# Kernel optimization log

Measured on AMD Instinct MI355X. Metric: run time of the kernel, lower is better.

Reference implementation:

```python
import jax, jax.numpy as jnp
import numpy as np
import math

B, N, T, H, HEADS, FIN, NL_TR = 4, 256, 16, 128, 4, 2, 5
M = B * N
NEG = -1e9

def _sinusoidal(t, h):
    pos = jnp.arange(t, dtype=jnp.float32)[:, None]
    div = jnp.exp(jnp.arange(0, h, 2, dtype=jnp.float32) * (-math.log(10000.0) / h))
    pe = jnp.zeros((t, h), dtype=jnp.float32)
    pe = pe.at[:, 0::2].set(jnp.sin(pos * div))
    pe = pe.at[:, 1::2].set(jnp.cos(pos * div))
    return pe

def _gat(x, W, a_src, a_dst, b, E, m):
    # x: [T,M,F]; W: [F,heads,H]; E: [T,M,M] bool, E[t,i,j]=edge j->i; m: [T,M] bool
    h = jnp.einsum('tmf,fhd->tmhd', x, W)
    ss = jnp.einsum('tmhd,hd->tmh', h, a_src)  # source score per node
    sd = jnp.einsum('tmhd,hd->tmh', h, a_dst)  # dest score per node
    logits = jax.nn.leaky_relu(sd[:, :, None, :] + ss[:, None, :, :], 0.2)  # [T,i,j,h]
    logits = jnp.where(E[..., None], logits, NEG)
    alpha = jax.nn.softmax(logits, axis=2)  # segment-softmax over incoming edges
    out = jnp.einsum('tijh,tjhd->tihd', alpha, h).mean(axis=2) + b  # concat=False -> head mean + bias
    return jax.nn.relu(out) * m[..., None]

def _ln(x, s, b):
    mu = x.mean(-1, keepdims=True)
    v = ((x - mu) ** 2).mean(-1, keepdims=True)
    return (x - mu) / jnp.sqrt(v + 1e-5) * s + b

def _forward(ego_mask, positions, adjacency, gat1_W, gat1_asrc, gat1_adst, gat1_b, gatW, gat_asrc, gat_adst, gat_b, Wqkv, bqkv, Wo, bo, ln1_s, ln1_b, ln2_s, ln2_b, Wff1, bff1, Wff2, bff2):
    m = jnp.transpose(ego_mask, (1, 0, 2)).reshape(T, M)  # [T, B*N]
    eye = jnp.eye(M, dtype=bool)
    # edge j->i valid iff A[t,j,i]!=0 and both nodes masked; PyG GATConv adds self-loops
    E = ((jnp.swapaxes(adjacency, 1, 2) != 0) & m[:, :, None] & m[:, None, :]) | (eye[None] & m[:, :, None])
    x = _gat(positions, gat1_W, gat1_asrc, gat1_adst, gat1_b, E, m)
    for i in range(5):
        x = _gat(x, gatW[i], gat_asrc[i], gat_adst[i], gat_b[i], E, m)
    x_seq = jnp.transpose(x, (1, 0, 2)) + _sinusoidal(T, H)[None]  # [M, T, H]
    dh = H // HEADS
    scale = 1.0 / math.sqrt(dh)
    for l in range(NL_TR):
        q = (x_seq @ Wqkv[l, 0] + bqkv[l, 0]).reshape(M, T, HEADS, dh)
        k = (x_seq @ Wqkv[l, 1] + bqkv[l, 1]).reshape(M, T, HEADS, dh)
        v = (x_seq @ Wqkv[l, 2] + bqkv[l, 2]).reshape(M, T, HEADS, dh)
        sc = jnp.einsum('bqhd,bkhd->bhqk', q, k) * scale
        a = jax.nn.softmax(sc, axis=-1)
        o = jnp.einsum('bhqk,bkhd->bqhd', a, v).reshape(M, T, H) @ Wo[l] + bo[l]
        x_seq = _ln(x_seq + o, ln1_s[l], ln1_b[l])
        f = jax.nn.relu(x_seq @ Wff1[l] + bff1[l]) @ Wff2[l] + bff2[l]
        x_seq = _ln(x_seq + f, ln2_s[l], ln2_b[l])
    return x_seq.reshape(B, N, T, H)

def setup_inputs() -> dict:
    key = jax.random.key(0)
    ks = jax.random.split(key, 32)
    s = 0.05
    f32 = jnp.float32
    inp = {
        'ego_mask': jax.random.uniform(ks[0], (B, T, N)) < 0.95,
        'positions': jax.random.normal(ks[1], (T, M, FIN), dtype=f32),
        'adjacency': (jax.random.uniform(ks[2], (T, M, M)) < 0.02).astype(f32),
        'gat1_W': jax.random.normal(ks[3], (FIN, HEADS, H), dtype=f32) * s,
        'gat1_asrc': jax.random.normal(ks[4], (HEADS, H), dtype=f32) * s,
        'gat1_adst': jax.random.normal(ks[5], (HEADS, H), dtype=f32) * s,
        'gat1_b': jnp.zeros((H,), dtype=f32),
        'gatW': jax.random.normal(ks[6], (5, H, HEADS, H), dtype=f32) * s,
        'gat_asrc': jax.random.normal(ks[7], (5, HEADS, H), dtype=f32) * s,
        'gat_adst': jax.random.normal(ks[8], (5, HEADS, H), dtype=f32) * s,
        'gat_b': jnp.zeros((5, H), dtype=f32),
        'Wqkv': jax.random.normal(ks[9], (NL_TR, 3, H, H), dtype=f32) * s,
        'bqkv': jnp.zeros((NL_TR, 3, H), dtype=f32),
        'Wo': jax.random.normal(ks[10], (NL_TR, H, H), dtype=f32) * s,
        'bo': jnp.zeros((NL_TR, H), dtype=f32),
        'ln1_s': jnp.ones((NL_TR, H), dtype=f32),
        'ln1_b': jnp.zeros((NL_TR, H), dtype=f32),
        'ln2_s': jnp.ones((NL_TR, H), dtype=f32),
        'ln2_b': jnp.zeros((NL_TR, H), dtype=f32),
        'Wff1': jax.random.normal(ks[11], (NL_TR, H, 4 * H), dtype=f32) * s,
        'bff1': jnp.zeros((NL_TR, 4 * H), dtype=f32),
        'Wff2': jax.random.normal(ks[12], (NL_TR, 4 * H, H), dtype=f32) * s,
        'bff2': jnp.zeros((NL_TR, H), dtype=f32),
    }
    return inp

def reference(ego_mask, positions, adjacency, gat1_W, gat1_asrc, gat1_adst, gat1_b, gatW, gat_asrc, gat_adst, gat_b, Wqkv, bqkv, Wo, bo, ln1_s, ln1_b, ln2_s, ln2_b, Wff1, bff1, Wff2, bff2):
    return _forward(ego_mask, positions, adjacency, gat1_W, gat1_asrc, gat1_adst, gat1_b, gatW, gat_asrc, gat_adst, gat_b, Wqkv, bqkv, Wo, bo, ln1_s, ln1_b, ln2_s, ln2_b, Wff1, bff1, Wff2, bff2)
```

## Files before the change

kernel.cpp:

```cpp
#include <hip/hip_runtime.h>
#include <hip/hip_bf16.h>

#define TT 16
#define MM 1024
#define HDIM 128
#define NHEADS 4
#define NROWS (TT*MM)
#define MAXDEG 64

typedef __bf16 bf16x8 __attribute__((ext_vector_type(8)));
typedef float f32x4 __attribute__((ext_vector_type(4)));

__device__ __forceinline__ unsigned short f2b(float x) {
    unsigned u = __float_as_uint(x);
    u += 0x7fff + ((u >> 16) & 1);
    return (unsigned short)(u >> 16);
}
__device__ __forceinline__ float bu2f(unsigned short u) {
    return __uint_as_float(((unsigned)u) << 16);
}
__device__ __forceinline__ void unpk8(uint4 v, float* f) {
    f[0] = bu2f((unsigned short)(v.x & 0xffff)); f[1] = bu2f((unsigned short)(v.x >> 16));
    f[2] = bu2f((unsigned short)(v.y & 0xffff)); f[3] = bu2f((unsigned short)(v.y >> 16));
    f[4] = bu2f((unsigned short)(v.z & 0xffff)); f[5] = bu2f((unsigned short)(v.z >> 16));
    f[6] = bu2f((unsigned short)(v.w & 0xffff)); f[7] = bu2f((unsigned short)(v.w >> 16));
}

__global__ __launch_bounds__(256) void k_init(const int* __restrict__ ego,
                                              float* __restrict__ mfl,
                                              int* __restrict__ cnt) {
    int idx = blockIdx.x * 256 + threadIdx.x;
    int t = idx >> 10, i = idx & 1023;
    int b = i >> 8, n = i & 255;
    mfl[idx] = ego[b * (TT * 256) + t * 256 + n] ? 1.f : 0.f;
    cnt[idx] = 0;
}

__global__ __launch_bounds__(256) void k_edges(const float* __restrict__ adj,
                                               const float* __restrict__ mfl,
                                               int* __restrict__ cnt,
                                               int* __restrict__ nbr) {
    int bid = blockIdx.x;
    int t = bid >> 6, jc = bid & 63;
    int tid = threadIdx.x;
    int i0 = tid * 4;
    int rowb = t * MM;
    float mi[4];
#pragma unroll
    for (int r = 0; r < 4; ++r) mi[r] = mfl[rowb + i0 + r];
    __shared__ float ms[16];
    if (tid < 16) ms[tid] = mfl[rowb + jc * 16 + tid];
    __syncthreads();
    const float* at = adj + (size_t)t * MM * MM;
#pragma unroll 4
    for (int jj = 0; jj < 16; ++jj) {
        int j = jc * 16 + jj;
        float4 a = *(const float4*)(at + (size_t)j * MM + i0);
        float mj = ms[jj];
#pragma unroll
        for (int r = 0; r < 4; ++r) {
            int i = i0 + r;
            bool e;
            if (j == i) e = (mi[r] != 0.f);
            else e = ((&a.x)[r] != 0.f) && (mj != 0.f) && (mi[r] != 0.f);
            if (e) {
                int row = rowb + i;
                int pos = atomicAdd(&cnt[row], 1);
                if (pos < MAXDEG) nbr[(size_t)row * MAXDEG + pos] = j;
            }
        }
    }
}

__global__ __launch_bounds__(256) void k_prep(const float* __restrict__ Wqkv,
                                              const float* __restrict__ Wo,
                                              const float* __restrict__ Wff1,
                                              const float* __restrict__ Wff2,
                                              const float* __restrict__ gW,
                                              unsigned short* __restrict__ Wb) {
    int o = blockIdx.x * 256 + threadIdx.x;
    const float* src; int cs;
    if (o < 122880) {
        int l = o / 24576, r = o % 24576;
        if (r < 6144) {
            int nt = r >> 8, rem = r & 255, ks = rem >> 6, lane = rem & 63;
            int mt = nt >> 3, cc = nt & 7;
            int k = ks * 32 + ((lane >> 4) << 3), c = cc * 16 + (lane & 15);
            src = Wqkv + ((size_t)(l * 3 + mt) * 128 + k) * 128 + c; cs = 128;
        } else if (r < 8192) {
            int u = r - 6144, nt = u >> 8, rem = u & 255, ks = rem >> 6, lane = rem & 63;
            int k = ks * 32 + ((lane >> 4) << 3), c = nt * 16 + (lane & 15);
            src = Wo + (size_t)l * 16384 + (size_t)k * 128 + c; cs = 128;
        } else if (r < 16384) {
            int u = r - 8192, nt = u >> 8, rem = u & 255, ks = rem >> 6, lane = rem & 63;
            int k = ks * 32 + ((lane >> 4) << 3), c = nt * 16 + (lane & 15);
            src = Wff1 + (size_t)l * 65536 + (size_t)k * 512 + c; cs = 512;
        } else {
            int u = r - 16384, nt = u >> 10, rem = u & 1023, ks = rem >> 6, lane = rem & 63;
            int k = ks * 32 + ((lane >> 4) << 3), c = nt * 16 + (lane & 15);
            src = Wff2 + (size_t)l * 65536 + (size_t)k * 128 + c; cs = 128;
        }
    } else {
        int u = o - 122880;
        int l = u >> 13, rr = u & 8191;
        int nt = rr >> 8, rem = rr & 255, ks = rem >> 6, lane = rem & 63;
        int k = ks * 32 + ((lane >> 4) << 3), c = nt * 16 + (lane & 15);
        src = gW + (size_t)l * 65536 + (size_t)k * 512 + c; cs = 512;
    }
    unsigned v[4];
#pragma unroll
    for (int j = 0; j < 4; ++j)
        v[j] = (unsigned)f2b(src[(2 * j) * (size_t)cs]) |
               ((unsigned)f2b(src[(2 * j + 1) * (size_t)cs]) << 16);
    *(uint4*)(Wb + (size_t)o * 8) = make_uint4(v[0], v[1], v[2], v[3]);
}

__global__ __launch_bounds__(128) void k_gat1(const float* __restrict__ x,
                                              const float* __restrict__ W,
                                              const float* __restrict__ asrc,
                                              const float* __restrict__ adst,
                                              unsigned short* __restrict__ h16,
                                              float* __restrict__ ss,
                                              float* __restrict__ sd) {
    int bid = blockIdx.x;
    int row = ((bid & 7) << 11) + (bid >> 3);
    int tid = threadIdx.x;
    float x0 = x[row * 2], x1 = x[row * 2 + 1];
    float s4[4], d4[4];
#pragma unroll
    for (int hh = 0; hh < 4; ++hh) {
        int o = hh * 128 + tid;
        float v = x0 * W[o] + x1 * W[512 + o];
        h16[(size_t)row * 512 + o] = f2b(v);
        s4[hh] = v * asrc[o];
        d4[hh] = v * adst[o];
    }
#pragma unroll
    for (int hh = 0; hh < 4; ++hh)
        for (int off = 32; off; off >>= 1) {
            s4[hh] += __shfl_down(s4[hh], off, 64);
            d4[hh] += __shfl_down(d4[hh], off, 64);
        }
    __shared__ float red[2][2][4];
    if ((tid & 63) == 0) {
        int w = tid >> 6;
#pragma unroll
        for (int hh = 0; hh < 4; ++hh) { red[w][0][hh] = s4[hh]; red[w][1][hh] = d4[hh]; }
    }
    __syncthreads();
    if (tid < 4) ss[row * 4 + tid] = red[0][0][tid] + red[1][0][tid];
    else if (tid < 8) sd[row * 4 + tid - 4] = red[0][1][tid - 4] + red[1][1][tid - 4];
}

__global__ __launch_bounds__(256) void k_gat_h(const unsigned short* __restrict__ x16,
                                               const unsigned short* __restrict__ Wg,
                                               const float* __restrict__ asrc,
                                               const float* __restrict__ adst,
                                               unsigned short* __restrict__ h16,
                                               float* __restrict__ ss,
                                               float* __restrict__ sd) {
    __shared__ __align__(16) unsigned short xb[16 * 136];
    int bid = blockIdx.x;
    int row0 = (((bid & 7) << 7) + (bid >> 3)) * 16;
    int tid = threadIdx.x;
    {
        int rr = tid >> 4, cc = (tid & 15) * 8;
        *(uint4*)(xb + rr * 136 + cc) = *(const uint4*)(x16 + (size_t)(row0 + rr) * 128 + cc);
    }
    __syncthreads();
    const int lane = tid & 63, w = tid >> 6;
    const int mrow = lane & 15, quad = lane >> 4;
    bf16x8 af[4];
#pragma unroll
    for (int ks = 0; ks < 4; ++ks)
        af[ks] = *(const bf16x8*)(xb + mrow * 136 + ks * 32 + quad * 8);
    f32x4 acc[8];
#pragma unroll
    for (int i = 0; i < 8; ++i) acc[i] = (f32x4){0.f, 0.f, 0.f, 0.f};
#pragma unroll
    for (int ib = 0; ib < 4; ++ib) {
        bf16x8 wb[8];
#pragma unroll
        for (int u = 0; u < 2; ++u) {
            int nt = w * 8 + ib * 2 + u;
#pragma unroll
            for (int ks = 0; ks < 4; ++ks)
                wb[u * 4 + ks] = *(const bf16x8*)(Wg + (size_t)((nt * 4 + ks) * 64 + lane) * 8);
        }
#pragma unroll
        for (int u = 0; u < 2; ++u)
#pragma unroll
            for (int ks = 0; ks < 4; ++ks)
                acc[ib * 2 + u] = __builtin_amdgcn_mfma_f32_16x16x32_bf16(af[ks], wb[u * 4 + ks], acc[ib * 2 + u], 0, 0, 0);
    }
    float ps[4] = {0, 0, 0, 0}, pd[4] = {0, 0, 0, 0};
#pragma unroll
    for (int i = 0; i < 8; ++i) {
        int nt = w * 8 + i, col = nt * 16 + mrow;
        float as_ = asrc[col], ad_ = adst[col];
#pragma unroll
        for (int r = 0; r < 4; ++r) {
            float v = acc[i][r];
            h16[(size_t)(row0 + quad * 4 + r) * 512 + col] = f2b(v);
            ps[r] += v * as_; pd[r] += v * ad_;
        }
    }
#pragma unroll
    for (int off = 1; off < 16; off <<= 1)
#pragma unroll
        for (int r = 0; r < 4; ++r) {
            ps[r] += __shfl_xor(ps[r], off, 64);
            pd[r] += __shfl_xor(pd[r], off, 64);
        }
    if (mrow == 0) {
#pragma unroll
        for (int r = 0; r < 4; ++r) {
            int row = row0 + quad * 4 + r;
            ss[row * 4 + w] = ps[r];
            sd[row * 4 + w] = pd[r];
        }
    }
}

__global__ __launch_bounds__(256) void k_agg(const unsigned short* __restrict__ h16,
                                             const float* __restrict__ ss,
                                             const float* __restrict__ sd,
                                             const int* __restrict__ cnt,
                                             const int* __restrict__ nbr,
                                             const float* __restrict__ mfl,
                                             const float* __restrict__ bias,
                                             unsigned short* __restrict__ xo16) {
    int bid = blockIdx.x;
    int row = ((bid & 7) << 11) + (bid >> 3);
    int tid = threadIdx.x;
    int t = row >> 10;
    if (mfl[row] == 0.f) { if (tid < 128) xo16[(size_t)row * 128 + tid] = 0; return; }
    int c = cnt[row]; if (c > MAXDEG) c = MAXDEG;
    __shared__ int nb[MAXDEG];
    __shared__ float al[MAXDEG][4];
    __shared__ __align__(16) float part[1024];
    if (tid < c) nb[tid] = nbr[(size_t)row * MAXDEG + tid];
    __syncthreads();
    for (int idx = tid; idx < c * 4; idx += 256) {
        int n = idx >> 2, hh = idx & 3, j = nb[n];
        float lg = sd[row * 4 + hh] + ss[(t * MM + j) * 4 + hh];
        al[n][hh] = lg > 0.f ? lg : 0.2f * lg;
    }
    __syncthreads();
    if (tid < 128) {
        int hh = tid >> 5, n0 = tid & 31;
        float v1 = (n0 < c) ? al[n0][hh] : -1e30f;
        float v2 = (n0 + 32 < c) ? al[n0 + 32][hh] : -1e30f;
        float mx = fmaxf(v1, v2);
#pragma unroll
        for (int off = 16; off; off >>= 1) mx = fmaxf(mx, __shfl_xor(mx, off, 32));
        float e1 = (n0 < c) ? __expf(v1 - mx) : 0.f;
        float e2 = (n0 + 32 < c) ? __expf(v2 - mx) : 0.f;
        float s = e1 + e2;
#pragma unroll
        for (int off = 16; off; off >>= 1) s += __shfl_xor(s, off, 32);
        float inv = 1.f / s;
        if (n0 < c) al[n0][hh] = e1 * inv;
        if (n0 + 32 < c) al[n0 + 32][hh] = e2 * inv;
    }
    __syncthreads();
    {
        int half = tid >> 7, ct = tid & 127;
        int hh2 = ct >> 5;
        float a0 = 0.f, a1 = 0.f, a2 = 0.f, a3 = 0.f;
        const unsigned short* hbase = h16 + (size_t)t * MM * 512 + ct * 4;
#pragma unroll 2
        for (int n = half; n < c; n += 2) {
            int j = nb[n];
            uint2 v = *(const uint2*)(hbase + (size_t)j * 512);
            float w = al[n][hh2];
            a0 += w * bu2f((unsigned short)(v.x & 0xffff));
            a1 += w * bu2f((unsigned short)(v.x >> 16));
            a2 += w * bu2f((unsigned short)(v.y & 0xffff));
            a3 += w * bu2f((unsigned short)(v.y >> 16));
        }
        *(float4*)(part + tid * 4) = make_float4(a0, a1, a2, a3);
    }
    __syncthreads();
    if (tid < 128) {
        float v = 0.25f * ((part[tid] + part[512 + tid]) + (part[128 + tid] + part[640 + tid]) +
                           (part[256 + tid] + part[768 + tid]) + (part[384 + tid] + part[896 + tid]))
                + bias[tid];
        xo16[(size_t)row * 128 + tid] = f2b(fmaxf(v, 0.f));
    }
}

__device__ __forceinline__ void ln256(float* xs, const float* s, const float* b) {
    int tid = threadIdx.x, row = tid >> 4, lane = tid & 15;
    float* xr = xs + row * 128;
    float sum = 0.f;
#pragma unroll
    for (int k2 = 0; k2 < 8; ++k2) sum += xr[lane + 16 * k2];
#pragma unroll
    for (int off = 8; off; off >>= 1) sum += __shfl_xor(sum, off, 16);
    float mean = sum * (1.f / 128.f);
    float vs = 0.f;
#pragma unroll
    for (int k2 = 0; k2 < 8; ++k2) { float d = xr[lane + 16 * k2] - mean; vs += d * d; }
#pragma unroll
    for (int off = 8; off; off >>= 1) vs += __shfl_xor(vs, off, 16);
    float rstd = rsqrtf(vs * (1.f / 128.f) + 1e-5f);
#pragma unroll
    for (int k2 = 0; k2 < 8; ++k2) {
        int d = lane + 16 * k2;
        float v = (xr[d] - mean) * rstd;
        xr[d] = v * s[d] + b[d];
    }
    __syncthreads();
}

__global__ __launch_bounds__(256, 2) void k_tf(const unsigned short* __restrict__ xg,
        const unsigned short* __restrict__ Wb,
        const float* __restrict__ bqkv, const float* __restrict__ bo,
        const float* __restrict__ ln1s, const float* __restrict__ ln1b,
        const float* __restrict__ ln2s, const float* __restrict__ ln2b,
        const float* __restrict__ bff1, const float* __restrict__ bff2,
        float* __restrict__ out) {
    __shared__ __align__(16) float smem[8320];
    float* xs = smem;
    float* sb = smem + 2048;
    unsigned short* xb16  = (unsigned short*)(smem + 3072);
    unsigned short* Qb16  = (unsigned short*)(smem + 4160);
    unsigned short* Kb16  = (unsigned short*)(smem + 5248);
    unsigned short* Vb16  = (unsigned short*)(smem + 6336);
    unsigned short* hid16 = (unsigned short*)(smem + 4160);
    const int m = blockIdx.x, tid = threadIdx.x;
    const int lane = tid & 63, w = tid >> 6;
    const int mrow = lane & 15, quad = lane >> 4;

    for (int idx = tid; idx < 2048; idx += 256) {
        int t = idx >> 7, d = idx & 127, jj = d >> 1;
        float arg = (float)t * expf(-(float)(2 * jj) * (9.210340371976184f / 128.f));
        float pe = (d & 1) ? cosf(arg) : sinf(arg);
        xs[idx] = bu2f(xg[(size_t)t * (MM * HDIM) + (size_t)m * HDIM + d]) + pe;
    }
    __syncthreads();

    const int crow = tid >> 4, ccb = (tid & 15) * 8;
    for (int l = 0; l < 5; ++l) {
        const unsigned short* Wl = Wb + (size_t)l * 196608;
        {
            const float* xp = xs + crow * 128 + ccb;
            unsigned v[4];
#pragma unroll
            for (int j = 0; j < 4; ++j)
                v[j] = (unsigned)f2b(xp[2 * j]) | ((unsigned)f2b(xp[2 * j + 1]) << 16);
            *(uint4*)(xb16 + crow * 136 + ccb) = make_uint4(v[0], v[1], v[2], v[3]);
        }
        __syncthreads();
        {
            bf16x8 af[4];
#pragma unroll
            for (int ks = 0; ks < 4; ++ks)
                af[ks] = *(const bf16x8*)(xb16 + mrow * 136 + ks * 32 + quad * 8);
            f32x4 acc[6];
#pragma unroll
            for (int i = 0; i < 6; ++i) acc[i] = (f32x4){0.f, 0.f, 0.f, 0.f};
#pragma unroll
            for (int ib = 0; ib < 3; ++ib) {
                bf16x8 wb[8];
#pragma unroll
                for (int u = 0; u < 2; ++u) {
                    int nt = w * 6 + ib * 2 + u;
                    const unsigned short* bp = Wl + (size_t)(nt * 4) * 512 + lane * 8;
#pragma unroll
                    for (int ks = 0; ks < 4; ++ks)
                        wb[u * 4 + ks] = *(const bf16x8*)(bp + ks * 512);
                }
#pragma unroll
                for (int u = 0; u < 2; ++u)
#pragma unroll
                    for (int ks = 0; ks < 4; ++ks)
                        acc[ib * 2 + u] = __builtin_amdgcn_mfma_f32_16x16x32_bf16(af[ks], wb[u * 4 + ks], acc[ib * 2 + u], 0, 0, 0);
            }
#pragma unroll
            for (int i = 0; i < 6; ++i) {
                int nt = w * 6 + i, mt = nt >> 3, cc = nt & 7;
                int col = cc * 16 + mrow;
                float bb = bqkv[l * 384 + mt * 128 + col];
                unsigned short* dst = (mt == 0) ? Qb16 : (mt == 1) ? Kb16 : Vb16;
#pragma unroll
                for (int r = 0; r < 4; ++r)
                    dst[(quad * 4 + r) * 136 + col] = f2b(acc[i][r] + bb);
            }
        }
        __syncthreads();
        {
            int hh = tid >> 6, tq = (tid >> 2) & 15, tk0 = (tid & 3) * 4;
            const unsigned short* qp = Qb16 + tq * 136 + hh * 32;
            float a[4] = {0.f, 0.f, 0.f, 0.f};
#pragma unroll
            for (int d4 = 0; d4 < 4; ++d4) {
                uint4 qv = *(const uint4*)(qp + d4 * 8);
                float qf[8]; unpk8(qv, qf);
#pragma unroll
                for (int j = 0; j < 4; ++j) {
                    uint4 kv = *(const uint4*)(Kb16 + (tk0 + j) * 136 + hh * 32 + d4 * 8);
                    float kf[8]; unpk8(kv, kf);
#pragma unroll
                    for (int e = 0; e < 8; ++e) a[j] += qf[e] * kf[e];
                }
            }
#pragma unroll
            for (int j = 0; j < 4; ++j)
                sb[(tk0 + j) * 64 + hh * 16 + tq] = a[j] * 0.17677669529663687f;
        }
        __syncthreads();
        if (tid < 64) {
            float mx = -1e30f;
#pragma unroll
            for (int u = 0; u < 16; ++u) mx = fmaxf(mx, sb[u * 64 + tid]);
            float s = 0.f;
#pragma unroll
            for (int u = 0; u < 16; ++u) { float e = __expf(sb[u * 64 + tid] - mx); sb[u * 64 + tid] = e; s += e; }
            float inv = 1.f / s;
#pragma unroll
            for (int u = 0; u < 16; ++u) sb[u * 64 + tid] *= inv;
        }
        __syncthreads();
        {
            int o = tid & 127, r0p = (tid >> 7) * 8, hh = o >> 5;
            float accp[8] = {0, 0, 0, 0, 0, 0, 0, 0};
            for (int u = 0; u < 16; ++u) {
                float vv = bu2f(Vb16[u * 136 + o]);
                const float* pp = sb + u * 64 + hh * 16 + r0p;
#pragma unroll
                for (int r = 0; r < 8; ++r) accp[r] += pp[r] * vv;
            }
#pragma unroll
            for (int r = 0; r < 8; ++r)
                xb16[(r0p + r) * 136 + o] = f2b(accp[r]);
        }
        __syncthreads();
        {
            bf16x8 af[4];
#pragma unroll
            for (int ks = 0; ks < 4; ++ks)
                af[ks] = *(const bf16x8*)(xb16 + mrow * 136 + ks * 32 + quad * 8);
            const unsigned short* Ws = Wl + 49152;
            bf16x8 wb[8];
#pragma unroll
            for (int u = 0; u < 2; ++u) {
                int nt = w * 2 + u;
#pragma unroll
                for (int ks = 0; ks < 4; ++ks)
                    wb[u * 4 + ks] = *(const bf16x8*)(Ws + (size_t)((nt * 4 + ks) * 64 + lane) * 8);
            }
            f32x4 acc[2];
            acc[0] = (f32x4){0.f, 0.f, 0.f, 0.f};
            acc[1] = (f32x4){0.f, 0.f, 0.f, 0.f};
#pragma unroll
            for (int u = 0; u < 2; ++u)
#pragma unroll
                for (int ks = 0; ks < 4; ++ks)
                    acc[u] = __builtin_amdgcn_mfma_f32_16x16x32_bf16(af[ks], wb[u * 4 + ks], acc[u], 0, 0, 0);
#pragma unroll
            for (int u = 0; u < 2; ++u) {
                int col = (w * 2 + u) * 16 + mrow;
                float bb = bo[l * 128 + col];
#pragma unroll
                for (int r = 0; r < 4; ++r)
                    xs[(quad * 4 + r) * 128 + col] += acc[u][r] + bb;
            }
        }
        __syncthreads();
        ln256(xs, ln1s + l * 128, ln1b + l * 128);
        {
            const float* xp = xs + crow * 128 + ccb;
            unsigned v[4];
#pragma unroll
            for (int j = 0; j < 4; ++j)
                v[j] = (unsigned)f2b(xp[2 * j]) | ((unsigned)f2b(xp[2 * j + 1]) << 16);
            *(uint4*)(xb16 + crow * 136 + ccb) = make_uint4(v[0], v[1], v[2], v[3]);
        }
        __syncthreads();
        {
            bf16x8 af[4];
#pragma unroll
            for (int ks = 0; ks < 4; ++ks)
                af[ks] = *(const bf16x8*)(xb16 + mrow * 136 + ks * 32 + quad * 8);
            f32x4 acc[8];
#pragma unroll
            for (int i = 0; i < 8; ++i) acc[i] = (f32x4){0.f, 0.f, 0.f, 0.f};
            const unsigned short* Ws = Wl + 65536;
#pragma unroll
            for (int ib = 0; ib < 4; ++ib) {
                bf16x8 wb[8];
#pragma unroll
                for (int u = 0; u < 2; ++u) {
                    int nt = w * 8 + ib * 2 + u;
#pragma unroll
                    for (int ks = 0; ks < 4; ++ks)
                        wb[u * 4 + ks] = *(const bf16x8*)(Ws + (size_t)((nt * 4 + ks) * 64 + lane) * 8);
                }
#pragma unroll
                for (int u = 0; u < 2; ++u)
#pragma unroll
                    for (int ks = 0; ks < 4; ++ks)
                        acc[ib * 2 + u] = __builtin_amdgcn_mfma_f32_16x16x32_bf16(af[ks], wb[u * 4 + ks], acc[ib * 2 + u], 0, 0, 0);
            }
#pragma unroll
            for (int i = 0; i < 8; ++i) {
                int col = (w * 8 + i) * 16 + mrow;
                float bb = bff1[l * 512 + col];
#pragma unroll
                for (int r = 0; r < 4; ++r) {
                    float v = fmaxf(acc[i][r] + bb, 0.f);
                    hid16[(quad * 4 + r) * 520 + col] = f2b(v);
                }
            }
        }
        __syncthreads();
        {
            f32x4 a0 = (f32x4){0.f, 0.f, 0.f, 0.f};
            f32x4 a1 = (f32x4){0.f, 0.f, 0.f, 0.f};
            const unsigned short* Ws = Wl + 131072;
            int nt0 = w * 2, nt1 = w * 2 + 1;
#pragma unroll
            for (int kb = 0; kb < 4; ++kb) {
                bf16x8 afb[4], w0[4], w1[4];
#pragma unroll
                for (int kk = 0; kk < 4; ++kk) {
                    int ks = kb * 4 + kk;
                    afb[kk] = *(const bf16x8*)(hid16 + mrow * 520 + ks * 32 + quad * 8);
                    w0[kk] = *(const bf16x8*)(Ws + (size_t)((nt0 * 16 + ks) * 64 + lane) * 8);
                    w1[kk] = *(const bf16x8*)(Ws + (size_t)((nt1 * 16 + ks) * 64 + lane) * 8);
                }
#pragma unroll
                for (int kk = 0; kk < 4; ++kk) {
                    a0 = __builtin_amdgcn_mfma_f32_16x16x32_bf16(afb[kk], w0[kk], a0, 0, 0, 0);
                    a1 = __builtin_amdgcn_mfma_f32_16x16x32_bf16(afb[kk], w1[kk], a1, 0, 0, 0);
                }
            }
            int col0 = nt0 * 16 + mrow, col1 = nt1 * 16 + mrow;
            float bb0 = bff2[l * 128 + col0], bb1 = bff2[l * 128 + col1];
#pragma unroll
            for (int r = 0; r < 4; ++r) {
                xs[(quad * 4 + r) * 128 + col0] += a0[r] + bb0;
                xs[(quad * 4 + r) * 128 + col1] += a1[r] + bb1;
            }
        }
        __syncthreads();
        ln256(xs, ln2s + l * 128, ln2b + l * 128);
    }
    for (int idx = tid; idx < 2048; idx += 256)
        out[(size_t)m * 2048 + idx] = xs[idx];
}

extern "C" void kernel_launch(void* const* d_in, const int* in_sizes, int n_in,
                              void* d_out, int out_size, void* d_ws, size_t ws_size,
                              hipStream_t stream) {
    (void)in_sizes; (void)n_in; (void)out_size; (void)ws_size;
    const int*   ego  = (const int*)d_in[0];
    const float* pos  = (const float*)d_in[1];
    const float* adj  = (const float*)d_in[2];
    const float* g1W  = (const float*)d_in[3];
    const float* g1as = (const float*)d_in[4];
    const float* g1ad = (const float*)d_in[5];
    const float* g1b  = (const float*)d_in[6];
    const float* gW   = (const float*)d_in[7];
    const float* gas  = (const float*)d_in[8];
    const float* gad  = (const float*)d_in[9];
    const float* gb   = (const float*)d_in[10];
    const float* Wqkv = (const float*)d_in[11];
    const float* bqkv = (const float*)d_in[12];
    const float* Wo   = (const float*)d_in[13];
    const float* bo   = (const float*)d_in[14];
    const float* l1s  = (const float*)d_in[15];
    const float* l1b  = (const float*)d_in[16];
    const float* l2s  = (const float*)d_in[17];
    const float* l2b  = (const float*)d_in[18];
    const float* Wff1 = (const float*)d_in[19];
    const float* bff1 = (const float*)d_in[20];
    const float* Wff2 = (const float*)d_in[21];
    const float* bff2 = (const float*)d_in[22];

    unsigned short* x0  = (unsigned short*)d_ws;
    unsigned short* x1  = x0 + 2097152;
    unsigned short* h16 = x1 + 2097152;
    float* ssb = (float*)(h16 + 8388608);
    float* sdb = ssb + 65536;
    float* mfl = sdb + 65536;
    int*   cnt = (int*)(mfl + 16384);
    int*   nbr = cnt + 16384;
    unsigned short* Wb16 = (unsigned short*)(nbr + 1048576);
    unsigned short* Wg16 = Wb16 + 983040;

    k_prep<<<640, 256, 0, stream>>>(Wqkv, Wo, Wff1, Wff2, gW, Wb16);
    k_init<<<64, 256, 0, stream>>>(ego, mfl, cnt);
    k_edges<<<1024, 256, 0, stream>>>(adj, mfl, cnt, nbr);

    k_gat1<<<NROWS, 128, 0, stream>>>(pos, g1W, g1as, g1ad, h16, ssb, sdb);
    k_agg<<<NROWS, 256, 0, stream>>>(h16, ssb, sdb, cnt, nbr, mfl, g1b, x0);

    unsigned short* xin = x0; unsigned short* xout = x1;
    for (int L = 0; L < 5; ++L) {
        k_gat_h<<<1024, 256, 0, stream>>>(xin, Wg16 + (size_t)L * 65536,
                                          gas + L * 512, gad + L * 512, h16, ssb, sdb);
        k_agg<<<NROWS, 256, 0, stream>>>(h16, ssb, sdb, cnt, nbr, mfl, gb + L * 128, xout);
        unsigned short* tmp = xin; xin = xout; xout = tmp;
    }

    k_tf<<<MM, 256, 0, stream>>>(xin, Wb16, bqkv, bo, l1s, l1b, l2s, l2b,
                                 bff1, bff2, (float*)d_out);
}
```

Measured before the change: 568.5 us.

## Aggregate four GAT rows per block with one wave each; double GAT row tile

k_agg now gives each row one wavefront, four rows per block. The softmax over neighbours is done in registers with wave shuffles, and each lane gathers 8 contiguous bf16 features per neighbour. This replaces the old one-row-per-256-thread block that needed several shared-memory passes and block barriers. k_gat_h now processes 32 rows per block instead of 16 and reuses each loaded weight fragment for two row groups, halving the weight traffic per row. The attention dot-product unpacking in the transformer kernel is inlined by hand, which is mostly cosmetic.

```diff
diff --git a/kernel.cpp b/kernel.cpp
--- a/kernel.cpp
+++ b/kernel.cpp
@@ -18,12 +18,6 @@
 }
 __device__ __forceinline__ float bu2f(unsigned short u) {
     return __uint_as_float(((unsigned)u) << 16);
-}
-__device__ __forceinline__ void unpk8(uint4 v, float* f) {
-    f[0] = bu2f((unsigned short)(v.x & 0xffff)); f[1] = bu2f((unsigned short)(v.x >> 16));
-    f[2] = bu2f((unsigned short)(v.y & 0xffff)); f[3] = bu2f((unsigned short)(v.y >> 16));
-    f[4] = bu2f((unsigned short)(v.z & 0xffff)); f[5] = bu2f((unsigned short)(v.z >> 16));
-    f[6] = bu2f((unsigned short)(v.w & 0xffff)); f[7] = bu2f((unsigned short)(v.w >> 16));
 }
 
 __global__ __launch_bounds__(256) void k_init(const int* __restrict__ ego,
@@ -152,31 +146,27 @@
     else if (tid < 8) sd[row * 4 + tid - 4] = red[0][1][tid - 4] + red[1][1][tid - 4];
 }
 
-__global__ __launch_bounds__(256) void k_gat_h(const unsigned short* __restrict__ x16,
-                                               const unsigned short* __restrict__ Wg,
-                                               const float* __restrict__ asrc,
-                                               const float* __restrict__ adst,
-                                               unsigned short* __restrict__ h16,
-                                               float* __restrict__ ss,
-                                               float* __restrict__ sd) {
-    __shared__ __align__(16) unsigned short xb[16 * 136];
+__global__ __launch_bounds__(256, 2) void k_gat_h(const unsigned short* __restrict__ x16,
+                                                  const unsigned short* __restrict__ Wg,
+                                                  const float* __restrict__ asrc,
+                                                  const float* __restrict__ adst,
+                                                  unsigned short* __restrict__ h16,
+                                                  float* __restrict__ ss,
+                                                  float* __restrict__ sd) {
+    __shared__ __align__(16) unsigned short xb[32 * 136];
     int bid = blockIdx.x;
-    int row0 = (((bid & 7) << 7) + (bid >> 3)) * 16;
+    int row0 = (((bid & 7) << 6) + (bid >> 3)) * 32;
     int tid = threadIdx.x;
-    {
-        int rr = tid >> 4, cc = (tid & 15) * 8;
+#pragma unroll
+    for (int q = 0; q < 2; ++q) {
+        int u = tid + q * 256;
+        int rr = u >> 4, cc = (u & 15) * 8;
         *(uint4*)(xb + rr * 136 + cc) = *(const uint4*)(x16 + (size_t)(row0 + rr) * 128 + cc);
     }
     __syncthreads();
     const int lane = tid & 63, w = tid >> 6;
     const int mrow = lane & 15, quad = lane >> 4;
-    bf16x8 af[4];
-#pragma unroll
-    for (int ks = 0; ks < 4; ++ks)
-        af[ks] = *(const bf16x8*)(xb + mrow * 136 + ks * 32 + quad * 8);
-    f32x4 acc[8];
-#pragma unroll
-    for (int i = 0; i < 8; ++i) acc[i] = (f32x4){0.f, 0.f, 0.f, 0.f};
+    float ps[2][4] = {{0,0,0,0},{0,0,0,0}}, pd[2][4] = {{0,0,0,0},{0,0,0,0}};
 #pragma unroll
     for (int ib = 0; ib < 4; ++ib) {
         bf16x8 wb[8];
@@ -188,105 +178,144 @@
                 wb[u * 4 + ks] = *(const bf16x8*)(Wg + (size_t)((nt * 4 + ks) * 64 + lane) * 8);
         }
 #pragma unroll
-        for (int u = 0; u < 2; ++u)
+        for (int rg = 0; rg < 2; ++rg) {
+            bf16x8 af[4];
 #pragma unroll
             for (int ks = 0; ks < 4; ++ks)
-                acc[ib * 2 + u] = __builtin_amdgcn_mfma_f32_16x16x32_bf16(af[ks], wb[u * 4 + ks], acc[ib * 2 + u], 0, 0, 0);
-    }
-    float ps[4] = {0, 0, 0, 0}, pd[4] = {0, 0, 0, 0};
-#pragma unroll
-    for (int i = 0; i < 8; ++i) {
-        int nt = w * 8 + i, col = nt * 16 + mrow;
-        float as_ = asrc[col], ad_ = adst[col];
-#pragma unroll
-        for (int r = 0; r < 4; ++r) {
-            float v = acc[i][r];
-            h16[(size_t)(row0 + quad * 4 + r) * 512 + col] = f2b(v);
-            ps[r] += v * as_; pd[r] += v * ad_;
+                af[ks] = *(const bf16x8*)(xb + (rg * 16 + mrow) * 136 + ks * 32 + quad * 8);
+            f32x4 acc[2];
+            acc[0] = (f32x4){0.f, 0.f, 0.f, 0.f};
+            acc[1] = (f32x4){0.f, 0.f, 0.f, 0.f};
+#pragma unroll
+            for (int u = 0; u < 2; ++u)
+#pragma unroll
+                for (int ks = 0; ks < 4; ++ks)
+                    acc[u] = __builtin_amdgcn_mfma_f32_16x16x32_bf16(af[ks], wb[u * 4 + ks], acc[u], 0, 0, 0);
+#pragma unroll
+            for (int u = 0; u < 2; ++u) {
+                int nt = w * 8 + ib * 2 + u, col = nt * 16 + mrow;
+                float as_ = asrc[col], ad_ = adst[col];
+#pragma unroll
+                for (int r = 0; r < 4; ++r) {
+                    float v = acc[u][r];
+                    h16[(size_t)(row0 + rg * 16 + quad * 4 + r) * 512 + col] = f2b(v);
+                    ps[rg][r] += v * as_; pd[rg][r] += v * ad_;
+                }
+            }
         }
     }
 #pragma unroll
     for (int off = 1; off < 16; off <<= 1)
 #pragma unroll
-        for (int r = 0; r < 4; ++r) {
-            ps[r] += __shfl_xor(ps[r], off, 64);
-            pd[r] += __shfl_xor(pd[r], off, 64);
-        }
+        for (int rg = 0; rg < 2; ++rg)
+#pragma unroll
+            for (int r = 0; r < 4; ++r) {
+                ps[rg][r] += __shfl_xor(ps[rg][r], off, 64);
+                pd[rg][r] += __shfl_xor(pd[rg][r], off, 64);
+            }
     if (mrow == 0) {
 #pragma unroll
-        for (int r = 0; r < 4; ++r) {
-            int row = row0 + quad * 4 + r;
-            ss[row * 4 + w] = ps[r];
-            sd[row * 4 + w] = pd[r];
-        }
-    }
-}
-
-__global__ __launch_bounds__(256) void k_agg(const unsigned short* __restrict__ h16,
-                                             const float* __restrict__ ss,
-                                             const float* __restrict__ sd,
-                                             const int* __restrict__ cnt,
-                                             const int* __restrict__ nbr,
-                                             const float* __restrict__ mfl,
-                                             const float* __restrict__ bias,
-                                             unsigned short* __restrict__ xo16) {
+        for (int rg = 0; rg < 2; ++rg)
+#pragma unroll
+            for (int r = 0; r < 4; ++r) {
+                int row = row0 + rg * 16 + quad * 4 + r;
+                ss[row * 4 + w] = ps[rg][r];
+                sd[row * 4 + w] = pd[rg][r];
+            }
+    }
+}
+
+__global__ __launch_bounds__(256, 2) void k_agg(const unsigned short* __restrict__ h16,
+                                                const float* __restrict__ ss,
+                                                const float* __restrict__ sd,
+                                                const int* __restrict__ cnt,
+                                                const int* __restrict__ nbr,
+                                                const float* __restrict__ mfl,
+                                                const float* __restrict__ bias,
+                                                unsigned short* __restrict__ xo16) {
+    __shared__ float alB[4][MAXDEG][4];
+    __shared__ int   nbB[4][MAXDEG];
+    __shared__ __align__(16) float partB[4][512];
     int bid = blockIdx.x;
-    int row = ((bid & 7) << 11) + (bid >> 3);
+    int row0 = (((bid & 7) << 9) + (bid >> 3)) * 4;
     int tid = threadIdx.x;
-    int t = row >> 10;
-    if (mfl[row] == 0.f) { if (tid < 128) xo16[(size_t)row * 128 + tid] = 0; return; }
-    int c = cnt[row]; if (c > MAXDEG) c = MAXDEG;
-    __shared__ int nb[MAXDEG];
-    __shared__ float al[MAXDEG][4];
-    __shared__ __align__(16) float part[1024];
-    if (tid < c) nb[tid] = nbr[(size_t)row * MAXDEG + tid];
+    const int w = tid >> 6, lane = tid & 63;
+    int row = row0 + w, t = row >> 10;
+    bool valid = mfl[row] != 0.f;
+    int c = 0;
+    if (valid) { c = cnt[row]; if (c > MAXDEG) c = MAXDEG; }
+    bool act = lane < c;
+    int jreg = 0;
+    float lg[4];
+    if (act) {
+        jreg = nbr[(size_t)row * MAXDEG + lane];
+        int jr = t * MM + jreg;
+#pragma unroll
+        for (int hh = 0; hh < 4; ++hh) {
+            float v = sd[row * 4 + hh] + ss[jr * 4 + hh];
+            lg[hh] = v > 0.f ? v : 0.2f * v;
+        }
+    } else {
+#pragma unroll
+        for (int hh = 0; hh < 4; ++hh) lg[hh] = -1e30f;
+    }
+    float mx[4];
+#pragma unroll
+    for (int hh = 0; hh < 4; ++hh) mx[hh] = lg[hh];
+#pragma unroll
+    for (int off = 32; off; off >>= 1)
+#pragma unroll
+        for (int hh = 0; hh < 4; ++hh) mx[hh] = fmaxf(mx[hh], __shfl_xor(mx[hh], off, 64));
+    float ev[4];
+#pragma unroll
+    for (int hh = 0; hh < 4; ++hh) ev[hh] = act ? __expf(lg[hh] - mx[hh]) : 0.f;
+    float sm[4];
+#pragma unroll
+    for (int hh = 0; hh < 4; ++hh) sm[hh] = ev[hh];
+#pragma unroll
+    for (int off = 32; off; off >>= 1)
+#pragma unroll
+        for (int hh = 0; hh < 4; ++hh) sm[hh] += __shfl_xor(sm[hh], off, 64);
+    if (act) {
+        float4 a4 = make_float4(ev[0] / sm[0], ev[1] / sm[1], ev[2] / sm[2], ev[3] / sm[3]);
+        *(float4*)&alB[w][lane][0] = a4;
+        nbB[w][lane] = jreg;
+    }
     __syncthreads();
-    for (int idx = tid; idx < c * 4; idx += 256) {
-        int n = idx >> 2, hh = idx & 3, j = nb[n];
-        float lg = sd[row * 4 + hh] + ss[(t * MM + j) * 4 + hh];
-        al[n][hh] = lg > 0.f ? lg : 0.2f * lg;
-    }
-    __syncthreads();
-    if (tid < 128) {
-        int hh = tid >> 5, n0 = tid & 31;
-        float v1 = (n0 < c) ? al[n0][hh] : -1e30f;
-        float v2 = (n0 + 32 < c) ? al[n0 + 32][hh] : -1e30f;
-        float mx = fmaxf(v1, v2);
-#pragma unroll
-        for (int off = 16; off; off >>= 1) mx = fmaxf(mx, __shfl_xor(mx, off, 32));
-        float e1 = (n0 < c) ? __expf(v1 - mx) : 0.f;
-        float e2 = (n0 + 32 < c) ? __expf(v2 - mx) : 0.f;
-        float s = e1 + e2;
-#pragma unroll
-        for (int off = 16; off; off >>= 1) s += __shfl_xor(s, off, 32);
-        float inv = 1.f / s;
-        if (n0 < c) al[n0][hh] = e1 * inv;
-        if (n0 + 32 < c) al[n0 + 32][hh] = e2 * inv;
-    }
+    const int head = lane >> 4;
+    float acc[8] = {0, 0, 0, 0, 0, 0, 0, 0};
+    const unsigned short* hb = h16 + (size_t)t * MM * 512 + lane * 8;
+    for (int n = 0; n < c; ++n) {
+        int j = nbB[w][n];
+        float a = alB[w][n][head];
+        uint4 v = *(const uint4*)(hb + (size_t)j * 512);
+        acc[0] += a * bu2f((unsigned short)(v.x & 0xffff));
+        acc[1] += a * bu2f((unsigned short)(v.x >> 16));
+        acc[2] += a * bu2f((unsigned short)(v.y & 0xffff));
+        acc[3] += a * bu2f((unsigned short)(v.y >> 16));
+        acc[4] += a * bu2f((unsigned short)(v.z & 0xffff));
+        acc[5] += a * bu2f((unsigned short)(v.z >> 16));
+        acc[6] += a * bu2f((unsigned short)(v.w & 0xffff));
+        acc[7] += a * bu2f((unsigned short)(v.w >> 16));
+    }
+    *(float4*)&partB[w][lane * 8]     = make_float4(acc[0], acc[1], acc[2], acc[3]);
+    *(float4*)&partB[w][lane * 8 + 4] = make_float4(acc[4], acc[5], acc[6], acc[7]);
     __syncthreads();
     {
-        int half = tid >> 7, ct = tid & 127;
-        int hh2 = ct >> 5;
-        float a0 = 0.f, a1 = 0.f, a2 = 0.f, a3 = 0.f;
-        const unsigned short* hbase = h16 + (size_t)t * MM * 512 + ct * 4;
-#pragma unroll 2
-        for (int n = half; n < c; n += 2) {
-            int j = nb[n];
-            uint2 v = *(const uint2*)(hbase + (size_t)j * 512);
-            float w = al[n][hh2];
-            a0 += w * bu2f((unsigned short)(v.x & 0xffff));
-            a1 += w * bu2f((unsigned short)(v.x >> 16));
-            a2 += w * bu2f((unsigned short)(v.y & 0xffff));
-            a3 += w * bu2f((unsigned short)(v.y >> 16));
-        }
-        *(float4*)(part + tid * 4) = make_float4(a0, a1, a2, a3);
-    }
-    __syncthreads();
-    if (tid < 128) {
-        float v = 0.25f * ((part[tid] + part[512 + tid]) + (part[128 + tid] + part[640 + tid]) +
-                           (part[256 + tid] + part[768 + tid]) + (part[384 + tid] + part[896 + tid]))
-                + bias[tid];
-        xo16[(size_t)row * 128 + tid] = f2b(fmaxf(v, 0.f));
+        int d0 = lane * 2;
+        unsigned outp = 0;
+#pragma unroll
+        for (int q = 0; q < 2; ++q) {
+            int d = d0 + q;
+            float v = 0.f;
+            if (valid) {
+                v = 0.25f * (partB[w][d] + partB[w][128 + d] + partB[w][256 + d] + partB[w][384 + d])
+                    + bias[d];
+                v = fmaxf(v, 0.f);
+            }
+            outp |= ((unsigned)f2b(v)) << (16 * q);
+        }
+        *(unsigned*)(xo16 + (size_t)row * 128 + d0) = outp;
     }
 }
 
@@ -397,13 +426,22 @@
 #pragma unroll
             for (int d4 = 0; d4 < 4; ++d4) {
                 uint4 qv = *(const uint4*)(qp + d4 * 8);
-                float qf[8]; unpk8(qv, qf);
+                float qf[8];
+                qf[0] = bu2f((unsigned short)(qv.x & 0xffff)); qf[1] = bu2f((unsigned short)(qv.x >> 16));
+                qf[2] = bu2f((unsigned short)(qv.y & 0xffff)); qf[3] = bu2f((unsigned short)(qv.y >> 16));
+                qf[4] = bu2f((unsigned short)(qv.z & 0xffff)); qf[5] = bu2f((unsigned short)(qv.z >> 16));
+                qf[6] = bu2f((unsigned short)(qv.w & 0xffff)); qf[7] = bu2f((unsigned short)(qv.w >> 16));
 #pragma unroll
                 for (int j = 0; j < 4; ++j) {
                     uint4 kv = *(const uint4*)(Kb16 + (tk0 + j) * 136 + hh * 32 + d4 * 8);
-                    float kf[8]; unpk8(kv, kf);
-#pragma unroll
-                    for (int e = 0; e < 8; ++e) a[j] += qf[e] * kf[e];
+                    a[j] += qf[0] * bu2f((unsigned short)(kv.x & 0xffff));
+                    a[j] += qf[1] * bu2f((unsigned short)(kv.x >> 16));
+                    a[j] += qf[2] * bu2f((unsigned short)(kv.y & 0xffff));
+                    a[j] += qf[3] * bu2f((unsigned short)(kv.y >> 16));
+                    a[j] += qf[4] * bu2f((unsigned short)(kv.z & 0xffff));
+                    a[j] += qf[5] * bu2f((unsigned short)(kv.z >> 16));
+                    a[j] += qf[6] * bu2f((unsigned short)(kv.w & 0xffff));
+                    a[j] += qf[7] * bu2f((unsigned short)(kv.w >> 16));
                 }
             }
 #pragma unroll
@@ -596,13 +634,13 @@
     k_edges<<<1024, 256, 0, stream>>>(adj, mfl, cnt, nbr);
 
     k_gat1<<<NROWS, 128, 0, stream>>>(pos, g1W, g1as, g1ad, h16, ssb, sdb);
-    k_agg<<<NROWS, 256, 0, stream>>>(h16, ssb, sdb, cnt, nbr, mfl, g1b, x0);
+    k_agg<<<4096, 256, 0, stream>>>(h16, ssb, sdb, cnt, nbr, mfl, g1b, x0);
 
     unsigned short* xin = x0; unsigned short* xout = x1;
     for (int L = 0; L < 5; ++L) {
-        k_gat_h<<<1024, 256, 0, stream>>>(xin, Wg16 + (size_t)L * 65536,
-                                          gas + L * 512, gad + L * 512, h16, ssb, sdb);
-        k_agg<<<NROWS, 256, 0, stream>>>(h16, ssb, sdb, cnt, nbr, mfl, gb + L * 128, xout);
+        k_gat_h<<<512, 256, 0, stream>>>(xin, Wg16 + (size_t)L * 65536,
+                                         gas + L * 512, gad + L * 512, h16, ssb, sdb);
+        k_agg<<<4096, 256, 0, stream>>>(h16, ssb, sdb, cnt, nbr, mfl, gb + L * 128, xout);
         unsigned short* tmp = xin; xin = xout; xout = tmp;
     }
 
```

After: 508.0 us. 10.6% less time.
